# Performance work log

Measured on AMD Instinct MI355X. Metric: run time of the kernel, lower is better.

Reference implementation:

```python
import jax, jax.numpy as jnp
import numpy as np

B, T, D, H, L = 2048, 100, 51, 128, 3  # batch, window, vars, latent, layers


def _lstm_cell(x, h, c, Wih, Whh, b):
    # PyTorch gate order: i, f, g, o. b = b_ih + b_hh (mathematically identical).
    g = x @ Wih.T + h @ Whh.T + b
    i, f, gg, o = jnp.split(g, 4, axis=-1)
    i = jax.nn.sigmoid(i)
    f = jax.nn.sigmoid(f)
    gg = jnp.tanh(gg)
    o = jax.nn.sigmoid(o)
    c_new = f * c + i * gg
    h_new = o * jnp.tanh(c_new)
    return h_new, c_new


def _run_layer(xs, Wih, Whh, b):
    # xs: [T, B, in]; returns full h sequence and final (h, c)
    bsz = xs.shape[1]
    h0 = jnp.zeros((bsz, H), xs.dtype)
    c0 = jnp.zeros((bsz, H), xs.dtype)

    def step(carry, x):
        h, c = carry
        h, c = _lstm_cell(x, h, c, Wih, Whh, b)
        return (h, c), h

    (hT, cT), hs = jax.lax.scan(step, (h0, c0), xs)
    return hs, hT, cT


def setup_inputs() -> dict:
    key = jax.random.key(0)
    ks = iter(jax.random.split(key, 32))
    s = 0.05

    def w(shape):
        return jax.random.normal(next(ks), shape, dtype=jnp.float32) * s

    inp = {"src": jax.random.normal(next(ks), (B, T, D), dtype=jnp.float32)}
    # encoder LSTM params (layer0 input=D, layers1-2 input=H)
    for l in range(L):
        din = D if l == 0 else H
        inp[f"eW{l}"] = w((4 * H, din))
        inp[f"eU{l}"] = w((4 * H, H))
        inp[f"eb{l}"] = w((4 * H,))
    # decoder LSTM params (same input sizes: input_size=input_dim)
    for l in range(L):
        din = D if l == 0 else H
        inp[f"dW{l}"] = w((4 * H, din))
        inp[f"dU{l}"] = w((4 * H, H))
        inp[f"db{l}"] = w((4 * H,))
    inp["fW"] = w((D, H))
    inp["fb"] = w((D,))
    return inp


def reference(src, eW0, eU0, eb0, eW1, eU1, eb1, eW2, eU2, eb2,
              dW0, dU0, db0, dW1, dU1, db1, dW2, dU2, db2, fW, fb):
    bsz, seq, dvar = src.shape
    xs = jnp.transpose(src, (1, 0, 2))  # [T, B, D]

    # ----- encoder: 3 stacked LSTM layers (dropout is identity at eval) -----
    enc = [(eW0, eU0, eb0), (eW1, eU1, eb1), (eW2, eU2, eb2)]
    hs_fin, cs_fin = [], []
    cur = xs
    for (Wih, Whh, b) in enc:
        cur, hT, cT = _run_layer(cur, Wih, Whh, b)
        hs_fin.append(hT)
        cs_fin.append(cT)

    dec = [(dW0, dU0, db0), (dW1, dU1, db1), (dW2, dU2, db2)]
    x0 = jnp.zeros((bsz, dvar), src.dtype)

    def dec_step(carry, _):
        x, (h0, h1, h2), (c0, c1, c2) = carry
        h0, c0 = _lstm_cell(x, h0, c0, *dec[0])
        h1, c1 = _lstm_cell(h0, h1, c1, *dec[1])
        h2, c2 = _lstm_cell(h1, h2, c2, *dec[2])
        pred = h2 @ fW.T + fb  # note: self.relu is defined but never applied
        return (pred, (h0, h1, h2), (c0, c1, c2)), pred

    carry0 = (x0, tuple(hs_fin), tuple(cs_fin))
    _, preds = jax.lax.scan(dec_step, carry0, None, length=seq)  # [T, B, D]

    # cat along time then reverse time axis (inv_idx)
    out = jnp.transpose(preds, (1, 0, 2))[:, ::-1, :]
    return out
```

## Files before the change

kernel.cpp:

```cpp
#include <hip/hip_runtime.h>
#include <stdint.h>

#define Tn 100
#define Dn 51
#define Hn 128
#define G4 512
#define BR 8
#define NWG 256
#define NTH 1024
#define RP 264

typedef unsigned int uint32;
typedef unsigned short u16;
typedef short s16x8 __attribute__((ext_vector_type(8)));
typedef float f32x4v __attribute__((ext_vector_type(4)));

__device__ __forceinline__ float rcp_(float x){ return __builtin_amdgcn_rcpf(x); }
__device__ __forceinline__ float sigm(float x){ return rcp_(1.f + __expf(-x)); }
__device__ __forceinline__ float tanh_(float x){ return 1.f - 2.f*rcp_(1.f + __expf(2.f*x)); }

__device__ __forceinline__ u16 f2bf(float f){
  uint32 u = __float_as_uint(f);
  return (u16)((u + 0x7fffu + ((u >> 16) & 1u)) >> 16);
}
__device__ __forceinline__ float bf2f(u16 u){ return __uint_as_float(((uint32)u)<<16); }

__device__ __forceinline__ void wr_xh(u16* __restrict__ xhA, int r, int k, float v){
  u16 h = f2bf(v);
  xhA[r*RP + k]     = h;
  xhA[(r+8)*RP + k] = f2bf(v - bf2f(h));
}

struct WP {
  const float* W[6];
  const float* U[6];
  const float* Bb[6];
  const float* fW;
  const float* fb;
};

#define PREP_TOTAL (6*131072 + 6*512 + 8192 + 64)
__global__ void prep_kernel(WP p, u16* __restrict__ wsw, float* __restrict__ bias,
                            float* __restrict__ fwt, float* __restrict__ fbw)
{
  int gid = blockIdx.x*256 + threadIdx.x;
  if (gid >= PREP_TOTAL) return;
  if (gid < 6*131072){
    int l = gid >> 17;
    int e = gid & 131071;
    int n    = e >> 12;
    int s    = (e >> 9) & 7;
    int lane = (e >> 3) & 63;
    int j    = e & 7;
    int k = s*32 + (lane >> 4)*8 + j;
    int c = n*16 + (lane & 15);
    int din = (l % 3 == 0) ? Dn : Hn;
    int K = din + Hn;
    u16 v = 0;
    if (k < K){
      float f = (k < din) ? p.W[l][(size_t)c*din + k] : p.U[l][(size_t)c*Hn + (k - din)];
      v = f2bf(f);
    }
    wsw[gid] = v;
  } else if (gid < 6*131072 + 6*512){
    int i = gid - 6*131072;
    bias[i] = p.Bb[i>>9][i & 511];
  } else if (gid < 6*131072 + 6*512 + 8192){
    int i = gid - (6*131072 + 6*512);
    int k = i >> 6, d = i & 63;
    fwt[i] = (d < Dn) ? p.fW[(size_t)d*Hn + k] : 0.f;
  } else {
    int d = gid - (6*131072 + 6*512 + 8192);
    fbw[d] = (d < Dn) ? p.fb[d] : 0.f;
  }
}

template<int S>
__device__ __forceinline__ void gemm_mfma(const u16* __restrict__ wsl,
                                          const float* __restrict__ blS,
                                          const u16* __restrict__ xhA,
                                          float* __restrict__ gates, int tid)
{
  const int wave = tid >> 6, lane = tid & 63;
  const int mrow = lane & 15, kgrp = lane >> 4;
  const int n0 = wave*2;
  const u16* bp0 = wsl + n0*4096 + lane*8;
  const int aoff = mrow*RP + kgrp*8;
  f32x4v acc0 = {0.f,0.f,0.f,0.f}, acc1 = {0.f,0.f,0.f,0.f};
  #pragma unroll 2
  for (int s=0; s<S; s++){
    s16x8 a  = *(const s16x8*)(xhA + aoff + s*32);
    s16x8 b0 = *(const s16x8*)(bp0 + s*512);
    s16x8 b1 = *(const s16x8*)(bp0 + 4096 + s*512);
    acc0 = __builtin_amdgcn_mfma_f32_16x16x32_bf16(a, b0, acc0, 0, 0, 0);
    acc1 = __builtin_amdgcn_mfma_f32_16x16x32_bf16(a, b1, acc1, 0, 0, 0);
  }
  #pragma unroll
  for (int v=0; v<4; v++){
    float l0 = __shfl_down(acc0[v], 32);
    float l1 = __shfl_down(acc1[v], 32);
    acc0[v] += l0;
    acc1[v] += l1;
  }
  if (kgrp < 2){
    int rb = kgrp*4;
    int c0g = n0*16 + mrow, c1g = c0g + 16;
    float bv0 = blS[c0g], bv1 = blS[c1g];
    #pragma unroll
    for (int v=0; v<4; v++){
      gates[(rb+v)*G4 + c0g] = acc0[v] + bv0;
      gates[(rb+v)*G4 + c1g] = acc1[v] + bv1;
    }
  }
}

__device__ __forceinline__ void activate2(const float* __restrict__ gates,
                                          float* __restrict__ h, float* __restrict__ c,
                                          u16* __restrict__ xh_self, int din_self,
                                          u16* __restrict__ xh_next, int tid)
{
  int r = tid >> 7, j = tid & 127;
  const float* g = gates + r*G4;
  float ig = sigm (g[j]);
  float fg = sigm (g[j + Hn]);
  float gg = tanh_(g[j + 2*Hn]);
  float og = sigm (g[j + 3*Hn]);
  int hi = r*Hn + j;
  float cn = fg*c[hi] + ig*gg;
  c[hi] = cn;
  float hv = og*tanh_(cn);
  if (h) h[hi] = hv;
  wr_xh(xh_self, r, din_self + j, hv);
  if (xh_next) wr_xh(xh_next, r, j, hv);
}

__device__ __forceinline__ void ld_src(const float* __restrict__ src, long b0, int t,
                                       int tid, float& sA, float& sB)
{
  int k = tid & 255;
  if (k < Dn){
    int r0 = tid >> 8;
    sA = src[((size_t)(b0+r0)*Tn + t)*Dn + k];
    sB = src[((size_t)(b0+r0+4)*Tn + t)*Dn + k];
  }
}
__device__ __forceinline__ void st_src(u16* __restrict__ xh0, int tid, float sA, float sB)
{
  int k = tid & 255;
  if (k < Dn){
    int r0 = tid >> 8;
    wr_xh(xh0, r0,   k, sA);
    wr_xh(xh0, r0+4, k, sB);
  }
}

__device__ __forceinline__ void proj_out(const float* __restrict__ h2,
                                         const float* __restrict__ fwtS,
                                         const float* __restrict__ fbwS,
                                         u16* __restrict__ xh0,
                                         float* __restrict__ out, long b0, int t, int tid)
{
  if (tid < 512){
    int r = tid >> 6, d = tid & 63;
    const float* h = h2 + r*Hn;
    float acc = 0.f;
    #pragma unroll 8
    for (int k=0;k<Hn;k++) acc += h[k] * fwtS[k*64 + d];
    if (d < Dn){
      float pv = acc + fbwS[d];
      out[((size_t)(b0+r)*Tn + (Tn-1-t))*Dn + d] = pv;
      wr_xh(xh0, r, d, pv);
    }
  }
}

__global__ __launch_bounds__(NTH, 4) void lstm_kernel(
    const float* __restrict__ src, const u16* __restrict__ wsw,
    const float* __restrict__ bias, const float* __restrict__ fwt,
    const float* __restrict__ fbw, float* __restrict__ out)
{
  __shared__ __align__(16) u16   xhA[3*16*RP];
  __shared__ __align__(16) float gates[BR*G4];
  __shared__ __align__(16) float hS[BR*Hn];
  __shared__ __align__(16) float cS[3*BR*Hn];
  __shared__ __align__(16) float fwtS[8192];
  __shared__ __align__(16) float biasS[6*G4];
  __shared__ __align__(16) float fbwS[64];

  const int tid = threadIdx.x;
  const long b0 = (long)blockIdx.x * BR;
  u16* xh0 = xhA;
  u16* xh1 = xhA + 16*RP;
  u16* xh2 = xhA + 32*RP;

  float sA = 0.f, sB = 0.f;

  ld_src(src, b0, 0, tid, sA, sB);
  for (int i=tid; i<8192; i+=NTH) fwtS[i] = fwt[i];
  for (int i=tid; i<6*G4; i+=NTH) biasS[i] = bias[i];
  if (tid < 64) fbwS[tid] = fbw[tid];
  for (int i=tid; i<3*16*RP; i+=NTH) xhA[i]=0;
  for (int i=tid; i<BR*Hn; i+=NTH)   hS[i]=0.f;
  for (int i=tid; i<3*BR*Hn; i+=NTH) cS[i]=0.f;
  __syncthreads();
  st_src(xh0, tid, sA, sB);
  __syncthreads();

  for (int t=0;t<Tn;t++){
    int tn = (t < Tn-1) ? t+1 : Tn-1;
    ld_src(src, b0, tn, tid, sA, sB);
    gemm_mfma<6>(wsw + 0*131072, biasS + 0*G4, xh0, gates, tid);
    __syncthreads();
    activate2(gates, nullptr, cS,         xh0, Dn, xh1, tid);
    if (t < Tn-1) st_src(xh0, tid, sA, sB);
    __syncthreads();

    gemm_mfma<8>(wsw + 1*131072, biasS + 1*G4, xh1, gates, tid);
    __syncthreads();
    activate2(gates, nullptr, cS + BR*Hn, xh1, Hn, xh2, tid);
    __syncthreads();

    gemm_mfma<8>(wsw + 2*131072, biasS + 2*G4, xh2, gates, tid);
    __syncthreads();
    activate2(gates, nullptr, cS + 2*BR*Hn, xh2, Hn, (u16*)nullptr, tid);
    __syncthreads();
  }

  {
    int r = tid >> 7, k = tid & 127;
    if (k < Dn){ xh0[r*RP + k] = 0; xh0[(r+8)*RP + k] = 0; }
  }
  __syncthreads();

  for (int t=0;t<Tn;t++){
    gemm_mfma<6>(wsw + 3*131072, biasS + 3*G4, xh0, gates, tid);
    __syncthreads();
    activate2(gates, nullptr, cS,         xh0, Dn, xh1, tid);
    __syncthreads();

    gemm_mfma<8>(wsw + 4*131072, biasS + 4*G4, xh1, gates, tid);
    __syncthreads();
    activate2(gates, nullptr, cS + BR*Hn, xh1, Hn, xh2, tid);
    __syncthreads();

    gemm_mfma<8>(wsw + 5*131072, biasS + 5*G4, xh2, gates, tid);
    __syncthreads();
    activate2(gates, hS, cS + 2*BR*Hn, xh2, Hn, (u16*)nullptr, tid);
    __syncthreads();

    proj_out(hS, fwtS, fbwS, xh0, out, b0, t, tid);
    __syncthreads();
  }
}

extern "C" void kernel_launch(void* const* d_in, const int* in_sizes, int n_in,
                              void* d_out, int out_size, void* d_ws, size_t ws_size,
                              hipStream_t stream)
{
  (void)in_sizes; (void)n_in; (void)out_size; (void)ws_size;
  const float* src = (const float*)d_in[0];
  WP p;
  for (int l=0;l<3;l++){
    p.W[l]    = (const float*)d_in[1  + 3*l];
    p.U[l]    = (const float*)d_in[2  + 3*l];
    p.Bb[l]   = (const float*)d_in[3  + 3*l];
    p.W[3+l]  = (const float*)d_in[10 + 3*l];
    p.U[3+l]  = (const float*)d_in[11 + 3*l];
    p.Bb[3+l] = (const float*)d_in[12 + 3*l];
  }
  p.fW = (const float*)d_in[19];
  p.fb = (const float*)d_in[20];

  u16*   wsw  = (u16*)d_ws;
  float* bias = (float*)((char*)d_ws + 6*131072*sizeof(u16));
  float* fwt  = bias + 6*512;
  float* fbw  = fwt + 8192;

  prep_kernel<<<(PREP_TOTAL + 255)/256, 256, 0, stream>>>(p, wsw, bias, fwt, fbw);
  lstm_kernel<<<NWG, NTH, 0, stream>>>(src, wsw, bias, fwt, fbw, (float*)d_out);
}
```

Before: 1.851 ms.

## Stream LSTM weights into an LDS ring via async DMA and fuse gate activation

Replaces the direct global weight reads in the per-layer GEMM with a three-slot LDS ring buffer filled by global_load_lds DMA three k-steps ahead, prefetching across layer boundaries. Each wave now computes all four gates for 16 hidden units, so the activation runs in registers, the cell state stays in registers, and the gates LDS round trip plus several barriers go away. The workgroup shrinks to 512 threads, and the output projection is rewritten to use a transposed, padded weight layout with vector loads. The risks are hand-written waitcnt and barrier ordering in the ring pipeline, and lower per-workgroup thread parallelism.

```diff
diff --git a/kernel.cpp b/kernel.cpp
--- a/kernel.cpp
+++ b/kernel.cpp
@@ -7,8 +7,9 @@
 #define G4 512
 #define BR 8
 #define NWG 256
-#define NTH 1024
+#define NTH 512
 #define RP 264
+#define SLOT 16384
 
 typedef unsigned int uint32;
 typedef unsigned short u16;
@@ -39,7 +40,8 @@
   const float* fb;
 };
 
-#define PREP_TOTAL (6*131072 + 6*512 + 8192 + 64)
+#define FWTE (64*132)
+#define PREP_TOTAL (6*131072 + 6*512 + FWTE + 64)
 __global__ void prep_kernel(WP p, u16* __restrict__ wsw, float* __restrict__ bias,
                             float* __restrict__ fwt, float* __restrict__ fbw)
 {
@@ -65,191 +67,206 @@
   } else if (gid < 6*131072 + 6*512){
     int i = gid - 6*131072;
     bias[i] = p.Bb[i>>9][i & 511];
-  } else if (gid < 6*131072 + 6*512 + 8192){
+  } else if (gid < 6*131072 + 6*512 + FWTE){
     int i = gid - (6*131072 + 6*512);
-    int k = i >> 6, d = i & 63;
-    fwt[i] = (d < Dn) ? p.fW[(size_t)d*Hn + k] : 0.f;
+    int d = i / 132, k = i % 132;
+    fwt[i] = (k < Hn && d < Dn) ? p.fW[(size_t)d*Hn + k] : 0.f;
   } else {
-    int d = gid - (6*131072 + 6*512 + 8192);
+    int d = gid - (6*131072 + 6*512 + FWTE);
     fbw[d] = (d < Dn) ? p.fb[d] : 0.f;
   }
 }
 
-template<int S>
-__device__ __forceinline__ void gemm_mfma(const u16* __restrict__ wsl,
-                                          const float* __restrict__ blS,
-                                          const u16* __restrict__ xhA,
-                                          float* __restrict__ gates, int tid)
-{
-  const int wave = tid >> 6, lane = tid & 63;
+__device__ __forceinline__ void dma_tile(const u16* __restrict__ ws, u16* __restrict__ dslot,
+                                         int n, int ts, int lane){
+  const u16* g = ws + (((size_t)(n*8 + ts)) << 9) + (lane << 3);
+  u16* l = dslot + (n << 9);
+  __builtin_amdgcn_global_load_lds((const __attribute__((address_space(1))) uint32*)g,
+                                   (__attribute__((address_space(3))) uint32*)l, 16, 0, 0);
+}
+
+__device__ __forceinline__ void bar_lds(){
+  asm volatile("s_waitcnt lgkmcnt(0)" ::: "memory");
+  __builtin_amdgcn_s_barrier();
+}
+
+template<int S, bool H2SW>
+__device__ __forceinline__ void layer_step(
+    u16* __restrict__ ring, const u16* __restrict__ xh_in,
+    const u16* __restrict__ wsCur, const u16* __restrict__ wsNext,
+    const f32x4v bia, float (&creg)[4],
+    u16* __restrict__ xh_self, int din_self, u16* __restrict__ xh_next,
+    float* __restrict__ h2S, int wave, int lane, int& slot)
+{
   const int mrow = lane & 15, kgrp = lane >> 4;
-  const int n0 = wave*2;
-  const u16* bp0 = wsl + n0*4096 + lane*8;
-  const int aoff = mrow*RP + kgrp*8;
-  f32x4v acc0 = {0.f,0.f,0.f,0.f}, acc1 = {0.f,0.f,0.f,0.f};
-  #pragma unroll 2
-  for (int s=0; s<S; s++){
-    s16x8 a  = *(const s16x8*)(xhA + aoff + s*32);
-    s16x8 b0 = *(const s16x8*)(bp0 + s*512);
-    s16x8 b1 = *(const s16x8*)(bp0 + 4096 + s*512);
-    acc0 = __builtin_amdgcn_mfma_f32_16x16x32_bf16(a, b0, acc0, 0, 0, 0);
-    acc1 = __builtin_amdgcn_mfma_f32_16x16x32_bf16(a, b1, acc1, 0, 0, 0);
+  const int j = (wave << 4) + mrow;
+  const bool hi = (kgrp < 2);
+  const int aoff = mrow*RP + (kgrp << 3);
+  f32x4v aI, aF, aG, aO;
+  {
+    float bI = hi ? bia[0] : 0.f, bF = hi ? bia[1] : 0.f;
+    float bG = hi ? bia[2] : 0.f, bO = hi ? bia[3] : 0.f;
+    aI = (f32x4v){bI,bI,bI,bI}; aF = (f32x4v){bF,bF,bF,bF};
+    aG = (f32x4v){bG,bG,bG,bG}; aO = (f32x4v){bO,bO,bO,bO};
+  }
+  #pragma unroll
+  for (int k=0; k<S; k++){
+    asm volatile("s_waitcnt vmcnt(8)" ::: "memory");
+    u16* sb = ring + slot*SLOT;
+    s16x8 a  = *(const s16x8*)(xh_in + aoff + k*32);
+    s16x8 b0 = *(const s16x8*)(sb + ((wave     ) << 9) + (lane << 3));
+    s16x8 b1 = *(const s16x8*)(sb + ((wave +  8) << 9) + (lane << 3));
+    s16x8 b2 = *(const s16x8*)(sb + ((wave + 16) << 9) + (lane << 3));
+    s16x8 b3 = *(const s16x8*)(sb + ((wave + 24) << 9) + (lane << 3));
+    asm volatile("s_waitcnt lgkmcnt(0)" ::: "memory");
+    __builtin_amdgcn_sched_barrier(0);
+    {
+      const int m = k + 3;
+      const u16* wsx = (m < S) ? wsCur : wsNext;
+      const int ts   = (m < S) ? m : (m - S);
+      dma_tile(wsx, sb, wave,      ts, lane);
+      dma_tile(wsx, sb, wave +  8, ts, lane);
+      dma_tile(wsx, sb, wave + 16, ts, lane);
+      dma_tile(wsx, sb, wave + 24, ts, lane);
+    }
+    aI = __builtin_amdgcn_mfma_f32_16x16x32_bf16(a, b0, aI, 0,0,0);
+    aF = __builtin_amdgcn_mfma_f32_16x16x32_bf16(a, b1, aF, 0,0,0);
+    aG = __builtin_amdgcn_mfma_f32_16x16x32_bf16(a, b2, aG, 0,0,0);
+    aO = __builtin_amdgcn_mfma_f32_16x16x32_bf16(a, b3, aO, 0,0,0);
+    slot = (slot == 2) ? 0 : slot + 1;
   }
   #pragma unroll
   for (int v=0; v<4; v++){
-    float l0 = __shfl_down(acc0[v], 32);
-    float l1 = __shfl_down(acc1[v], 32);
-    acc0[v] += l0;
-    acc1[v] += l1;
-  }
-  if (kgrp < 2){
-    int rb = kgrp*4;
-    int c0g = n0*16 + mrow, c1g = c0g + 16;
-    float bv0 = blS[c0g], bv1 = blS[c1g];
+    aI[v] += __shfl_down(aI[v], 32);
+    aF[v] += __shfl_down(aF[v], 32);
+    aG[v] += __shfl_down(aG[v], 32);
+    aO[v] += __shfl_down(aO[v], 32);
+  }
+  float hvv[4];
+  if (hi){
     #pragma unroll
     for (int v=0; v<4; v++){
-      gates[(rb+v)*G4 + c0g] = acc0[v] + bv0;
-      gates[(rb+v)*G4 + c1g] = acc1[v] + bv1;
-    }
-  }
-}
-
-__device__ __forceinline__ void activate2(const float* __restrict__ gates,
-                                          float* __restrict__ h, float* __restrict__ c,
-                                          u16* __restrict__ xh_self, int din_self,
-                                          u16* __restrict__ xh_next, int tid)
-{
-  int r = tid >> 7, j = tid & 127;
-  const float* g = gates + r*G4;
-  float ig = sigm (g[j]);
-  float fg = sigm (g[j + Hn]);
-  float gg = tanh_(g[j + 2*Hn]);
-  float og = sigm (g[j + 3*Hn]);
-  int hi = r*Hn + j;
-  float cn = fg*c[hi] + ig*gg;
-  c[hi] = cn;
-  float hv = og*tanh_(cn);
-  if (h) h[hi] = hv;
-  wr_xh(xh_self, r, din_self + j, hv);
-  if (xh_next) wr_xh(xh_next, r, j, hv);
-}
-
-__device__ __forceinline__ void ld_src(const float* __restrict__ src, long b0, int t,
-                                       int tid, float& sA, float& sB)
-{
-  int k = tid & 255;
-  if (k < Dn){
-    int r0 = tid >> 8;
-    sA = src[((size_t)(b0+r0)*Tn + t)*Dn + k];
-    sB = src[((size_t)(b0+r0+4)*Tn + t)*Dn + k];
-  }
-}
-__device__ __forceinline__ void st_src(u16* __restrict__ xh0, int tid, float sA, float sB)
-{
-  int k = tid & 255;
-  if (k < Dn){
-    int r0 = tid >> 8;
-    wr_xh(xh0, r0,   k, sA);
-    wr_xh(xh0, r0+4, k, sB);
-  }
-}
-
-__device__ __forceinline__ void proj_out(const float* __restrict__ h2,
+      float iv = sigm (aI[v]);
+      float fv = sigm (aF[v]);
+      float gv = tanh_(aG[v]);
+      float ov = sigm (aO[v]);
+      creg[v] = fv*creg[v] + iv*gv;
+      float hv = ov*tanh_(creg[v]);
+      hvv[v] = hv;
+      int r = (kgrp << 2) + v;
+      if (xh_next) wr_xh(xh_next, r, j, hv);
+      if (H2SW)    h2S[r*Hn + j] = hv;
+    }
+  }
+  bar_lds();
+  if (hi){
+    #pragma unroll
+    for (int v=0; v<4; v++) wr_xh(xh_self, (kgrp<<2)+v, din_self + j, hvv[v]);
+  }
+}
+
+__device__ __forceinline__ void proj_out(const float* __restrict__ h2S,
                                          const float* __restrict__ fwtS,
                                          const float* __restrict__ fbwS,
                                          u16* __restrict__ xh0,
                                          float* __restrict__ out, long b0, int t, int tid)
 {
-  if (tid < 512){
-    int r = tid >> 6, d = tid & 63;
-    const float* h = h2 + r*Hn;
-    float acc = 0.f;
-    #pragma unroll 8
-    for (int k=0;k<Hn;k++) acc += h[k] * fwtS[k*64 + d];
-    if (d < Dn){
-      float pv = acc + fbwS[d];
-      out[((size_t)(b0+r)*Tn + (Tn-1-t))*Dn + d] = pv;
-      wr_xh(xh0, r, d, pv);
-    }
-  }
-}
-
-__global__ __launch_bounds__(NTH, 4) void lstm_kernel(
+  int r = tid >> 6, d = tid & 63;
+  const float* h = h2S + r*Hn;
+  const float* wrow = fwtS + d*132;
+  float acc = 0.f;
+  #pragma unroll
+  for (int kk=0; kk<Hn; kk+=4){
+    f32x4v w4 = *(const f32x4v*)(wrow + kk);
+    acc += h[kk]*w4[0] + h[kk+1]*w4[1] + h[kk+2]*w4[2] + h[kk+3]*w4[3];
+  }
+  if (d < Dn){
+    float pv = acc + fbwS[d];
+    out[((size_t)(b0+r)*Tn + (Tn-1-t))*Dn + d] = pv;
+    wr_xh(xh0, r, d, pv);
+  }
+}
+
+__global__ __launch_bounds__(NTH, 2) void lstm_kernel(
     const float* __restrict__ src, const u16* __restrict__ wsw,
     const float* __restrict__ bias, const float* __restrict__ fwt,
     const float* __restrict__ fbw, float* __restrict__ out)
 {
+  __shared__ __align__(16) u16   ring[3*SLOT];
   __shared__ __align__(16) u16   xhA[3*16*RP];
-  __shared__ __align__(16) float gates[BR*G4];
-  __shared__ __align__(16) float hS[BR*Hn];
-  __shared__ __align__(16) float cS[3*BR*Hn];
-  __shared__ __align__(16) float fwtS[8192];
-  __shared__ __align__(16) float biasS[6*G4];
+  __shared__ __align__(16) float fwtS[FWTE];
+  __shared__ __align__(16) float h2S[BR*Hn];
   __shared__ __align__(16) float fbwS[64];
 
   const int tid = threadIdx.x;
+  const int wave = tid >> 6, lane = tid & 63;
   const long b0 = (long)blockIdx.x * BR;
   u16* xh0 = xhA;
   u16* xh1 = xhA + 16*RP;
   u16* xh2 = xhA + 32*RP;
 
-  float sA = 0.f, sB = 0.f;
-
-  ld_src(src, b0, 0, tid, sA, sB);
-  for (int i=tid; i<8192; i+=NTH) fwtS[i] = fwt[i];
-  for (int i=tid; i<6*G4; i+=NTH) biasS[i] = bias[i];
+  const u16* wsE0 = wsw;
+  const u16* wsE1 = wsw + 1*131072;
+  const u16* wsE2 = wsw + 2*131072;
+  const u16* wsD0 = wsw + 3*131072;
+  const u16* wsD1 = wsw + 4*131072;
+  const u16* wsD2 = wsw + 5*131072;
+
+  float c0[4] = {0,0,0,0}, c1[4] = {0,0,0,0}, c2[4] = {0,0,0,0};
+  const int j = (wave << 4) + (lane & 15);
+  #define LDB(l) (f32x4v){ bias[(l)*G4 + j], bias[(l)*G4 + 128 + j], \
+                           bias[(l)*G4 + 256 + j], bias[(l)*G4 + 384 + j] }
+  f32x4v bE0 = LDB(0), bE1 = LDB(1), bE2 = LDB(2);
+  f32x4v bD0 = LDB(3), bD1 = LDB(4), bD2 = LDB(5);
+  #undef LDB
+
+  float sV = 0.f;
+  { int r = tid >> 6, k = tid & 63;
+    if (k < Dn) sV = src[((size_t)(b0+r)*Tn + 0)*Dn + k]; }
+
+  for (int i=tid; i<FWTE; i+=NTH) fwtS[i] = fwt[i];
   if (tid < 64) fbwS[tid] = fbw[tid];
-  for (int i=tid; i<3*16*RP; i+=NTH) xhA[i]=0;
-  for (int i=tid; i<BR*Hn; i+=NTH)   hS[i]=0.f;
-  for (int i=tid; i<3*BR*Hn; i+=NTH) cS[i]=0.f;
+  for (int i=tid; i<3*16*RP; i+=NTH) xhA[i] = 0;
   __syncthreads();
-  st_src(xh0, tid, sA, sB);
+  { int r = tid >> 6, k = tid & 63;
+    if (k < Dn) wr_xh(xh0, r, k, sV); }
   __syncthreads();
+
+  #pragma unroll
+  for (int ts=0; ts<3; ts++){
+    u16* db = ring + ts*SLOT;
+    dma_tile(wsE0, db, wave,      ts, lane);
+    dma_tile(wsE0, db, wave +  8, ts, lane);
+    dma_tile(wsE0, db, wave + 16, ts, lane);
+    dma_tile(wsE0, db, wave + 24, ts, lane);
+  }
+  int slot = 0;
 
   for (int t=0;t<Tn;t++){
     int tn = (t < Tn-1) ? t+1 : Tn-1;
-    ld_src(src, b0, tn, tid, sA, sB);
-    gemm_mfma<6>(wsw + 0*131072, biasS + 0*G4, xh0, gates, tid);
-    __syncthreads();
-    activate2(gates, nullptr, cS,         xh0, Dn, xh1, tid);
-    if (t < Tn-1) st_src(xh0, tid, sA, sB);
-    __syncthreads();
-
-    gemm_mfma<8>(wsw + 1*131072, biasS + 1*G4, xh1, gates, tid);
-    __syncthreads();
-    activate2(gates, nullptr, cS + BR*Hn, xh1, Hn, xh2, tid);
-    __syncthreads();
-
-    gemm_mfma<8>(wsw + 2*131072, biasS + 2*G4, xh2, gates, tid);
-    __syncthreads();
-    activate2(gates, nullptr, cS + 2*BR*Hn, xh2, Hn, (u16*)nullptr, tid);
-    __syncthreads();
-  }
-
-  {
-    int r = tid >> 7, k = tid & 127;
-    if (k < Dn){ xh0[r*RP + k] = 0; xh0[(r+8)*RP + k] = 0; }
-  }
-  __syncthreads();
+    { int r = tid >> 6, k = tid & 63;
+      if (k < Dn) sV = src[((size_t)(b0+r)*Tn + tn)*Dn + k]; }
+    layer_step<6,false>(ring, xh0, wsE0, wsE1, bE0, c0, xh0, Dn, xh1, h2S, wave, lane, slot);
+    layer_step<8,false>(ring, xh1, wsE1, wsE2, bE1, c1, xh1, Hn, xh2, h2S, wave, lane, slot);
+    if (t < Tn-1){
+      int r = tid >> 6, k = tid & 63;
+      if (k < Dn) wr_xh(xh0, r, k, sV);
+    }
+    layer_step<8,false>(ring, xh2, wsE2, (t < Tn-1) ? wsE0 : wsD0, bE2, c2,
+                        xh2, Hn, (u16*)nullptr, h2S, wave, lane, slot);
+  }
+
+  { int r = tid >> 6, k = tid & 63;
+    if (k < Dn){ xh0[r*RP + k] = 0; xh0[(r+8)*RP + k] = 0; } }
+  bar_lds();
 
   for (int t=0;t<Tn;t++){
-    gemm_mfma<6>(wsw + 3*131072, biasS + 3*G4, xh0, gates, tid);
-    __syncthreads();
-    activate2(gates, nullptr, cS,         xh0, Dn, xh1, tid);
-    __syncthreads();
-
-    gemm_mfma<8>(wsw + 4*131072, biasS + 4*G4, xh1, gates, tid);
-    __syncthreads();
-    activate2(gates, nullptr, cS + BR*Hn, xh1, Hn, xh2, tid);
-    __syncthreads();
-
-    gemm_mfma<8>(wsw + 5*131072, biasS + 5*G4, xh2, gates, tid);
-    __syncthreads();
-    activate2(gates, hS, cS + 2*BR*Hn, xh2, Hn, (u16*)nullptr, tid);
-    __syncthreads();
-
-    proj_out(hS, fwtS, fbwS, xh0, out, b0, t, tid);
-    __syncthreads();
+    layer_step<6,false>(ring, xh0, wsD0, wsD1, bD0, c0, xh0, Dn, xh1, h2S, wave, lane, slot);
+    layer_step<8,false>(ring, xh1, wsD1, wsD2, bD1, c1, xh1, Hn, xh2, h2S, wave, lane, slot);
+    layer_step<8,true >(ring, xh2, wsD2, wsD0, bD2, c2, xh2, Hn, (u16*)nullptr,
+                        h2S, wave, lane, slot);
+    proj_out(h2S, fwtS, fbwS, xh0, out, b0, t, tid);
+    bar_lds();
   }
 }
 
@@ -274,7 +291,7 @@
   u16*   wsw  = (u16*)d_ws;
   float* bias = (float*)((char*)d_ws + 6*131072*sizeof(u16));
   float* fwt  = bias + 6*512;
-  float* fbw  = fwt + 8192;
+  float* fbw  = fwt + FWTE;
 
   prep_kernel<<<(PREP_TOTAL + 255)/256, 256, 0, stream>>>(p, wsw, bias, fwt, fbw);
   lstm_kernel<<<NWG, NTH, 0, stream>>>(src, wsw, bias, fwt, fbw, (float*)d_out);
```

After: 2.452 ms. +32.5%, slower.
